# Kernel tuning notes

Hardware: AMD Instinct MI355X
Metric: run time of the kernel (lower is better)

The kernel has to match this reference:

```python
import jax, jax.numpy as jnp
import numpy as np

GAMMA = 0.99
ENTROPY_COEF = 0.01
GAE_LAMBDA = 0.95
VALUE_LOSS_COEF = 0.5

T = 65536          # agent rollout length
O, S, A = 8, 1048576, 6  # opponents, steps, actions


def setup_inputs() -> dict:
    key = jax.random.key(0)
    ks = jax.random.split(key, 9)
    return {
        "agent_rewards": jax.random.normal(ks[0], (T,), jnp.float32),
        "agent_log_probs": jax.random.normal(ks[1], (T,), jnp.float32),
        "agent_values": jax.random.normal(ks[2], (T + 1,), jnp.float32),
        "agent_entropies": jax.random.uniform(ks[3], (T,), jnp.float32),
        "opponent_log_probs": jax.random.normal(ks[4], (O, S, A), jnp.float32),
        "opponent_actions_ground_truths": jax.random.randint(ks[5], (O, S), 0, A),
        "opponent_values": jax.random.normal(ks[6], (O, S), jnp.float32),
        "opponent_rewards": jax.random.normal(ks[7], (O, S - 1), jnp.float32),
        "opponent_coefs": jax.random.uniform(ks[8], (O,), jnp.float32),
    }


def _agent_loss(rewards, values, log_probs, entropies):
    # Sequential GAE / discounted-return recurrence, scanned from last step to first.
    def step(carry, xs):
        R, gae, pl, vl = carry
        r, v, v_next, lp, ent = xs
        R = GAMMA * R + r
        adv = R - v
        vl = vl + 0.5 * adv * adv
        delta = r + GAMMA * v_next - v
        gae = gae * GAMMA * GAE_LAMBDA + delta
        pl = pl - lp * jax.lax.stop_gradient(gae) - ENTROPY_COEF * ent
        return (R, gae, pl, vl), None

    init = (values[-1], jnp.float32(0.0), jnp.float32(0.0), jnp.float32(0.0))
    xs = (rewards, values[:-1], values[1:], log_probs, entropies)
    (_, _, pl, vl), _ = jax.lax.scan(step, init, xs, reverse=True)
    return pl + VALUE_LOSS_COEF * vl


def _opponent_loss(log_probs, actions, values, rewards, coefs):
    # cross_entropy in torch applies log_softmax to its input, even though the arg
    # is (mis)named log_probs -> ce = mean(logsumexp(logits) - logits[target])
    logZ = jax.nn.logsumexp(log_probs, axis=-1)                      # (O, S)
    tgt = jnp.take_along_axis(log_probs, actions[..., None], axis=-1)[..., 0]
    ce = jnp.mean(logZ - tgt, axis=-1)                               # (O,)
    policy_loss = coefs * ce

    v0 = values[:, :-1]                                              # (O, S-1)
    v_next = values[:, 1:]                                           # roll(-1) then truncate
    pred = rewards + GAMMA * v_next
    d = v0 - pred
    ad = jnp.abs(d)
    sl1 = jnp.mean(jnp.where(ad < 1.0, 0.5 * d * d, ad - 0.5), axis=-1)
    value_loss = coefs * sl1
    return jnp.sum(policy_loss + value_loss)


def reference(agent_rewards, agent_log_probs, agent_values, agent_entropies,
              opponent_log_probs, opponent_actions_ground_truths,
              opponent_values, opponent_rewards, opponent_coefs):
    agent_loss = _agent_loss(agent_rewards, agent_values, agent_log_probs, agent_entropies)
    opp_loss = _opponent_loss(opponent_log_probs, opponent_actions_ground_truths,
                              opponent_values, opponent_rewards, opponent_coefs)
    return jnp.sum(agent_loss + opp_loss)
```

## Files before the change

### kernel.cpp

```cpp
#include <hip/hip_runtime.h>
#include <cstddef>

constexpr float GAMMA = 0.99f;
constexpr float GLAM  = 0.99f * 0.95f;
constexpr float ENT_C = 0.01f;

constexpr int T = 65536;
constexpr int O = 8;
constexpr int S = 1048576;
constexpr int BLK = 256;

constexpr int BPO        = 512;
constexpr int OPP_BLOCKS = O * BPO;
constexpr int ROWS_PER_B = S / BPO;
constexpr int CHUNK      = T / BLK;

typedef float f4 __attribute__((ext_vector_type(4)));
typedef int   i4 __attribute__((ext_vector_type(4)));

template <typename Tp>
__device__ __forceinline__ Tp ntload(const Tp* p) { return __builtin_nontemporal_load(p); }


__device__ __forceinline__ float row_ce(float l0, float l1, float l2,
                                        float l3, float l4, float l5, int a)
{
    float m  = fmaxf(fmaxf(fmaxf(l0, l1), fmaxf(l2, l3)), fmaxf(l4, l5));
    float se = __expf(l0 - m) + __expf(l1 - m) + __expf(l2 - m) +
               __expf(l3 - m) + __expf(l4 - m) + __expf(l5 - m);
    float tgt = (a == 0) ? l0 : (a == 1) ? l1 : (a == 2) ? l2 :
                (a == 3) ? l3 : (a == 4) ? l4 : l5;
    return (m + __logf(se)) - tgt;
}

__device__ __forceinline__ float sl1(float v0, float v1, float rw)
{
    float d  = v0 - (rw + GAMMA * v1);
    float ad = fabsf(d);
    return (ad < 1.f) ? 0.5f * d * d : ad - 0.5f;
}

__global__ __launch_bounds__(BLK)
void fused_kernel(const float* __restrict__ arew,
                  const float* __restrict__ alp,
                  const float* __restrict__ aval,
                  const float* __restrict__ aent,
                  const float* __restrict__ olp,
                  const int*   __restrict__ oact,
                  const float* __restrict__ oval,
                  const float* __restrict__ orew,
                  float* __restrict__ ws)
{
    const int tid = threadIdx.x;
    __shared__ float s1[BLK], s2[BLK];

    if (blockIdx.x == 0) {
        const int base = tid * CHUNK;

        float cR = 0.f, cG = 0.f;
        float nextv = aval[base + CHUNK];
        #pragma unroll 4
        for (int k4 = CHUNK - 4; k4 >= 0; k4 -= 4) {
            float4 r4 = *reinterpret_cast<const float4*>(&arew[base + k4]);
            float4 v4 = *reinterpret_cast<const float4*>(&aval[base + k4]);
            cR = GAMMA * cR + r4.w;  cG = GLAM * cG + (r4.w + GAMMA * nextv - v4.w);
            cR = GAMMA * cR + r4.z;  cG = GLAM * cG + (r4.z + GAMMA * v4.w  - v4.z);
            cR = GAMMA * cR + r4.y;  cG = GLAM * cG + (r4.y + GAMMA * v4.z  - v4.y);
            cR = GAMMA * cR + r4.x;  cG = GLAM * cG + (r4.x + GAMMA * v4.y  - v4.x);
            nextv = v4.x;
        }
        s1[tid] = cR; s2[tid] = cG;
        __syncthreads();

        if (tid == 0) {
            double aRd = 1.0, aGd = 1.0;
            for (int i = 0; i < CHUNK; ++i) { aRd *= 0.99; aGd *= 0.99 * 0.95; }
            const float aR = (float)aRd, aG = (float)aGd;
            float Rin = aval[T];
            float Gin = 0.f;
            for (int i = BLK - 1; i >= 0; --i) {
                float cr = s1[i], cg = s2[i];
                s1[i] = Rin; s2[i] = Gin;
                Rin = aR * Rin + cr;
                Gin = aG * Gin + cg;
            }
        }
        __syncthreads();
        float R = s1[tid], g = s2[tid];
        __syncthreads();

        float pl = 0.f, vl = 0.f;
        nextv = aval[base + CHUNK];
        #pragma unroll 4
        for (int k4 = CHUNK - 4; k4 >= 0; k4 -= 4) {
            float4 r4 = *reinterpret_cast<const float4*>(&arew[base + k4]);
            float4 v4 = *reinterpret_cast<const float4*>(&aval[base + k4]);
            float4 l4 = *reinterpret_cast<const float4*>(&alp [base + k4]);
            float4 e4 = *reinterpret_cast<const float4*>(&aent[base + k4]);

            R = GAMMA * R + r4.w; { float adv = R - v4.w; vl += 0.5f * adv * adv; }
            g = GLAM * g + (r4.w + GAMMA * nextv - v4.w); pl += -l4.w * g - ENT_C * e4.w;
            R = GAMMA * R + r4.z; { float adv = R - v4.z; vl += 0.5f * adv * adv; }
            g = GLAM * g + (r4.z + GAMMA * v4.w  - v4.z); pl += -l4.z * g - ENT_C * e4.z;
            R = GAMMA * R + r4.y; { float adv = R - v4.y; vl += 0.5f * adv * adv; }
            g = GLAM * g + (r4.y + GAMMA * v4.z  - v4.y); pl += -l4.y * g - ENT_C * e4.y;
            R = GAMMA * R + r4.x; { float adv = R - v4.x; vl += 0.5f * adv * adv; }
            g = GLAM * g + (r4.x + GAMMA * v4.y  - v4.x); pl += -l4.x * g - ENT_C * e4.x;
            nextv = v4.x;
        }
        s1[tid] = pl; s2[tid] = vl;
        __syncthreads();
        for (int stp = BLK / 2; stp > 0; stp >>= 1) {
            if (tid < stp) { s1[tid] += s1[tid + stp]; s2[tid] += s2[tid + stp]; }
            __syncthreads();
        }
        if (tid == 0) ws[2 * OPP_BLOCKS] = s1[0] + 0.5f * s2[0];
        return;
    }

    const int bid  = blockIdx.x - 1;
    const int o    = bid >> 9;
    const int seg  = bid & (BPO - 1);
    const int row0 = seg * ROWS_PER_B;
    const size_t obase = (size_t)o * S;
    const size_t rbase = (size_t)o * (S - 1);

    const int r1 = row0 + 4 * tid;
    const int r2 = row0 + (ROWS_PER_B / 2) + 4 * tid;

    const f4* Lp1 = reinterpret_cast<const f4*>(olp + (obase + r1) * 6);
    const f4* Lp2 = reinterpret_cast<const f4*>(olp + (obase + r2) * 6);
    f4 a0 = ntload(Lp1 + 0), a1 = ntload(Lp1 + 1), a2 = ntload(Lp1 + 2);
    f4 a3 = ntload(Lp1 + 3), a4 = ntload(Lp1 + 4), a5 = ntload(Lp1 + 5);
    f4 b0 = ntload(Lp2 + 0), b1 = ntload(Lp2 + 1), b2 = ntload(Lp2 + 2);
    f4 b3 = ntload(Lp2 + 3), b4 = ntload(Lp2 + 4), b5 = ntload(Lp2 + 5);

    i4 A1 = ntload(reinterpret_cast<const i4*>(oact + obase + r1));
    i4 A2 = ntload(reinterpret_cast<const i4*>(oact + obase + r2));
    f4 V1 = ntload(reinterpret_cast<const f4*>(oval + obase + r1));
    f4 V2 = ntload(reinterpret_cast<const f4*>(oval + obase + r2));
    float V1e = oval[obase + r1 + 4];
    float V2e = (r2 + 4 <= S - 1) ? oval[obase + r2 + 4] : 0.f;
    float w10 = ntload(orew + rbase + r1);
    float w11 = ntload(orew + rbase + r1 + 1);
    float w12 = ntload(orew + rbase + r1 + 2);
    float w13 = ntload(orew + rbase + r1 + 3);
    float w20 = ntload(orew + rbase + r2);
    float w21 = ntload(orew + rbase + r2 + 1);
    float w22 = ntload(orew + rbase + r2 + 2);
    float w23 = (r2 + 3 < S - 1) ? orew[rbase + r2 + 3] : 0.f;

    float ce_acc = 0.f, sl_acc = 0.f;

    ce_acc += row_ce(a0[0], a0[1], a0[2], a0[3], a1[0], a1[1], A1[0]);
    ce_acc += row_ce(a1[2], a1[3], a2[0], a2[1], a2[2], a2[3], A1[1]);
    ce_acc += row_ce(a3[0], a3[1], a3[2], a3[3], a4[0], a4[1], A1[2]);
    ce_acc += row_ce(a4[2], a4[3], a5[0], a5[1], a5[2], a5[3], A1[3]);
    ce_acc += row_ce(b0[0], b0[1], b0[2], b0[3], b1[0], b1[1], A2[0]);
    ce_acc += row_ce(b1[2], b1[3], b2[0], b2[1], b2[2], b2[3], A2[1]);
    ce_acc += row_ce(b3[0], b3[1], b3[2], b3[3], b4[0], b4[1], A2[2]);
    ce_acc += row_ce(b4[2], b4[3], b5[0], b5[1], b5[2], b5[3], A2[3]);

    sl_acc += sl1(V1[0], V1[1], w10);
    sl_acc += sl1(V1[1], V1[2], w11);
    sl_acc += sl1(V1[2], V1[3], w12);
    sl_acc += sl1(V1[3], V1e,   w13);
    sl_acc += sl1(V2[0], V2[1], w20);
    sl_acc += sl1(V2[1], V2[2], w21);
    sl_acc += sl1(V2[2], V2[3], w22);
    if (r2 + 3 < S - 1) sl_acc += sl1(V2[3], V2e, w23);

    s1[tid] = ce_acc; s2[tid] = sl_acc;
    __syncthreads();
    for (int stp = BLK / 2; stp > 0; stp >>= 1) {
        if (tid < stp) { s1[tid] += s1[tid + stp]; s2[tid] += s2[tid + stp]; }
        __syncthreads();
    }
    if (tid == 0) {
        ws[bid]              = s1[0];
        ws[OPP_BLOCKS + bid] = s2[0];
    }
}

__global__ __launch_bounds__(BLK)
void finalize_kernel(const float* __restrict__ ws,
                     const float* __restrict__ coefs,
                     float* __restrict__ out)
{
    const int tid = threadIdx.x;
    __shared__ float r1[BLK], r2[BLK];
    float tot = 0.f;
    for (int o = 0; o < O; ++o) {
        const float* cw = ws + o * BPO;
        const float* sw = ws + OPP_BLOCKS + o * BPO;
        r1[tid] = cw[tid] + cw[tid + BLK];
        r2[tid] = sw[tid] + sw[tid + BLK];
        __syncthreads();
        for (int stp = BLK / 2; stp > 0; stp >>= 1) {
            if (tid < stp) { r1[tid] += r1[tid + stp]; r2[tid] += r2[tid + stp]; }
            __syncthreads();
        }
        if (tid == 0)
            tot += coefs[o] * (r1[0] / (float)S + r2[0] / (float)(S - 1));
        __syncthreads();
    }
    if (tid == 0) out[0] = tot + ws[2 * OPP_BLOCKS];
}

extern "C" void kernel_launch(void* const* d_in, const int* in_sizes, int n_in,
                              void* d_out, int out_size, void* d_ws, size_t ws_size,
                              hipStream_t stream)
{
    const float* arew  = (const float*)d_in[0];
    const float* alp   = (const float*)d_in[1];
    const float* aval  = (const float*)d_in[2];
    const float* aent  = (const float*)d_in[3];
    const float* olp   = (const float*)d_in[4];
    const int*   oact  = (const int*)  d_in[5];
    const float* oval  = (const float*)d_in[6];
    const float* orew  = (const float*)d_in[7];
    const float* ocoef = (const float*)d_in[8];
    float* ws = (float*)d_ws;

    fused_kernel<<<1 + OPP_BLOCKS, BLK, 0, stream>>>(arew, alp, aval, aent,
                                                     olp, oact, oval, orew, ws);
    finalize_kernel<<<1, BLK, 0, stream>>>(ws, ocoef, (float*)d_out);
}
```

Before: 118.9 us.

## Switch opponent loss to grid-stride loop over row pairs with fused coefficient scaling

Replaces the fixed 4096-block layout (each thread handling two strips of four rows) with 2047 blocks running a grid-stride loop where each thread processes two adjacent rows per iteration. The per-opponent coefficient is applied inside the main kernel, so the finalize kernel becomes a single flat reduction over the per-block partials. The aim is less tail/launch overhead and a cheaper finalize. In exchange, accesses per iteration are narrower (float2, 3 float4s), the nontemporal load hints are dropped, and there is a per-row branch for the last step.

```diff
diff --git a/kernel.cpp b/kernel.cpp
--- a/kernel.cpp
+++ b/kernel.cpp
@@ -10,16 +10,11 @@
 constexpr int S = 1048576;
 constexpr int BLK = 256;
 
-constexpr int BPO        = 512;
-constexpr int OPP_BLOCKS = O * BPO;
-constexpr int ROWS_PER_B = S / BPO;
-constexpr int CHUNK      = T / BLK;
+constexpr int OPPB   = 2047;
+constexpr int NPAIRS = O * S / 2;
+constexpr int CHUNK  = T / BLK;
 
 typedef float f4 __attribute__((ext_vector_type(4)));
-typedef int   i4 __attribute__((ext_vector_type(4)));
-
-template <typename Tp>
-__device__ __forceinline__ Tp ntload(const Tp* p) { return __builtin_nontemporal_load(p); }
 
 
 __device__ __forceinline__ float row_ce(float l0, float l1, float l2,
@@ -49,6 +44,7 @@
                   const int*   __restrict__ oact,
                   const float* __restrict__ oval,
                   const float* __restrict__ orew,
+                  const float* __restrict__ ocoef,
                   float* __restrict__ ws)
 {
     const int tid = threadIdx.x;
@@ -114,61 +110,40 @@
             if (tid < stp) { s1[tid] += s1[tid + stp]; s2[tid] += s2[tid + stp]; }
             __syncthreads();
         }
-        if (tid == 0) ws[2 * OPP_BLOCKS] = s1[0] + 0.5f * s2[0];
+        if (tid == 0) ws[4096] = s1[0] + 0.5f * s2[0];
         return;
     }
 
-    const int bid  = blockIdx.x - 1;
-    const int o    = bid >> 9;
-    const int seg  = bid & (BPO - 1);
-    const int row0 = seg * ROWS_PER_B;
-    const size_t obase = (size_t)o * S;
-    const size_t rbase = (size_t)o * (S - 1);
-
-    const int r1 = row0 + 4 * tid;
-    const int r2 = row0 + (ROWS_PER_B / 2) + 4 * tid;
-
-    const f4* Lp1 = reinterpret_cast<const f4*>(olp + (obase + r1) * 6);
-    const f4* Lp2 = reinterpret_cast<const f4*>(olp + (obase + r2) * 6);
-    f4 a0 = ntload(Lp1 + 0), a1 = ntload(Lp1 + 1), a2 = ntload(Lp1 + 2);
-    f4 a3 = ntload(Lp1 + 3), a4 = ntload(Lp1 + 4), a5 = ntload(Lp1 + 5);
-    f4 b0 = ntload(Lp2 + 0), b1 = ntload(Lp2 + 1), b2 = ntload(Lp2 + 2);
-    f4 b3 = ntload(Lp2 + 3), b4 = ntload(Lp2 + 4), b5 = ntload(Lp2 + 5);
-
-    i4 A1 = ntload(reinterpret_cast<const i4*>(oact + obase + r1));
-    i4 A2 = ntload(reinterpret_cast<const i4*>(oact + obase + r2));
-    f4 V1 = ntload(reinterpret_cast<const f4*>(oval + obase + r1));
-    f4 V2 = ntload(reinterpret_cast<const f4*>(oval + obase + r2));
-    float V1e = oval[obase + r1 + 4];
-    float V2e = (r2 + 4 <= S - 1) ? oval[obase + r2 + 4] : 0.f;
-    float w10 = ntload(orew + rbase + r1);
-    float w11 = ntload(orew + rbase + r1 + 1);
-    float w12 = ntload(orew + rbase + r1 + 2);
-    float w13 = ntload(orew + rbase + r1 + 3);
-    float w20 = ntload(orew + rbase + r2);
-    float w21 = ntload(orew + rbase + r2 + 1);
-    float w22 = ntload(orew + rbase + r2 + 2);
-    float w23 = (r2 + 3 < S - 1) ? orew[rbase + r2 + 3] : 0.f;
+    const int bid    = blockIdx.x - 1;
+    const int gtid   = bid * BLK + tid;
+    const int stride = OPPB * BLK;
 
     float ce_acc = 0.f, sl_acc = 0.f;
 
-    ce_acc += row_ce(a0[0], a0[1], a0[2], a0[3], a1[0], a1[1], A1[0]);
-    ce_acc += row_ce(a1[2], a1[3], a2[0], a2[1], a2[2], a2[3], A1[1]);
-    ce_acc += row_ce(a3[0], a3[1], a3[2], a3[3], a4[0], a4[1], A1[2]);
-    ce_acc += row_ce(a4[2], a4[3], a5[0], a5[1], a5[2], a5[3], A1[3]);
-    ce_acc += row_ce(b0[0], b0[1], b0[2], b0[3], b1[0], b1[1], A2[0]);
-    ce_acc += row_ce(b1[2], b1[3], b2[0], b2[1], b2[2], b2[3], A2[1]);
-    ce_acc += row_ce(b3[0], b3[1], b3[2], b3[3], b4[0], b4[1], A2[2]);
-    ce_acc += row_ce(b4[2], b4[3], b5[0], b5[1], b5[2], b5[3], A2[3]);
+    for (int p = gtid; p < NPAIRS; p += stride) {
+        const int rr   = 2 * p;
+        const int o    = rr >> 20;
+        const int srel = rr & (S - 1);
+        const float coef = ocoef[o];
 
-    sl_acc += sl1(V1[0], V1[1], w10);
-    sl_acc += sl1(V1[1], V1[2], w11);
-    sl_acc += sl1(V1[2], V1[3], w12);
-    sl_acc += sl1(V1[3], V1e,   w13);
-    sl_acc += sl1(V2[0], V2[1], w20);
-    sl_acc += sl1(V2[1], V2[2], w21);
-    sl_acc += sl1(V2[2], V2[3], w22);
-    if (r2 + 3 < S - 1) sl_acc += sl1(V2[3], V2e, w23);
+        const f4* Lp = reinterpret_cast<const f4*>(olp) + (size_t)p * 3;
+        f4 q0 = Lp[0], q1 = Lp[1], q2 = Lp[2];
+        int2   ac  = *reinterpret_cast<const int2*>(oact + rr);
+        float2 v01 = *reinterpret_cast<const float2*>(oval + rr);
+
+        const bool last = (srel == S - 2);
+        float v2  = last ? 0.f : oval[rr + 2];
+        float rw0 = orew[rr - o];
+        float rw1 = last ? 0.f : orew[rr - o + 1];
+
+        float ce = row_ce(q0[0], q0[1], q0[2], q0[3], q1[0], q1[1], ac.x)
+                 + row_ce(q1[2], q1[3], q2[0], q2[1], q2[2], q2[3], ac.y);
+        float sl = sl1(v01.x, v01.y, rw0);
+        if (!last) sl += sl1(v01.y, v2, rw1);
+
+        ce_acc += coef * ce;
+        sl_acc += coef * sl;
+    }
 
     s1[tid] = ce_acc; s2[tid] = sl_acc;
     __syncthreads();
@@ -177,34 +152,29 @@
         __syncthreads();
     }
     if (tid == 0) {
-        ws[bid]              = s1[0];
-        ws[OPP_BLOCKS + bid] = s2[0];
+        ws[bid]        = s1[0];
+        ws[2048 + bid] = s2[0];
     }
 }
 
 __global__ __launch_bounds__(BLK)
-void finalize_kernel(const float* __restrict__ ws,
-                     const float* __restrict__ coefs,
-                     float* __restrict__ out)
+void finalize_kernel(const float* __restrict__ ws, float* __restrict__ out)
 {
     const int tid = threadIdx.x;
     __shared__ float r1[BLK], r2[BLK];
-    float tot = 0.f;
-    for (int o = 0; o < O; ++o) {
-        const float* cw = ws + o * BPO;
-        const float* sw = ws + OPP_BLOCKS + o * BPO;
-        r1[tid] = cw[tid] + cw[tid + BLK];
-        r2[tid] = sw[tid] + sw[tid + BLK];
-        __syncthreads();
-        for (int stp = BLK / 2; stp > 0; stp >>= 1) {
-            if (tid < stp) { r1[tid] += r1[tid + stp]; r2[tid] += r2[tid + stp]; }
-            __syncthreads();
-        }
-        if (tid == 0)
-            tot += coefs[o] * (r1[0] / (float)S + r2[0] / (float)(S - 1));
+    float c = 0.f, s = 0.f;
+    for (int i = tid; i < OPPB; i += BLK) {
+        c += ws[i];
+        s += ws[2048 + i];
+    }
+    r1[tid] = c; r2[tid] = s;
+    __syncthreads();
+    for (int stp = BLK / 2; stp > 0; stp >>= 1) {
+        if (tid < stp) { r1[tid] += r1[tid + stp]; r2[tid] += r2[tid + stp]; }
         __syncthreads();
     }
-    if (tid == 0) out[0] = tot + ws[2 * OPP_BLOCKS];
+    if (tid == 0)
+        out[0] = r1[0] / (float)S + r2[0] / (float)(S - 1) + ws[4096];
 }
 
 extern "C" void kernel_launch(void* const* d_in, const int* in_sizes, int n_in,
@@ -222,7 +192,7 @@
     const float* ocoef = (const float*)d_in[8];
     float* ws = (float*)d_ws;
 
-    fused_kernel<<<1 + OPP_BLOCKS, BLK, 0, stream>>>(arew, alp, aval, aent,
-                                                     olp, oact, oval, orew, ws);
-    finalize_kernel<<<1, BLK, 0, stream>>>(ws, ocoef, (float*)d_out);
+    fused_kernel<<<1 + OPPB, BLK, 0, stream>>>(arew, alp, aval, aent,
+                                               olp, oact, oval, orew, ocoef, ws);
+    finalize_kernel<<<1, BLK, 0, stream>>>(ws, (float*)d_out);
 }
```

After: 125.8 us. +5.8%, slower.
